# Performance work log

Measured on AMD Instinct MI355X. Metric: run time of the kernel, lower is better.

The kernel has to match this reference:

```python
import jax, jax.numpy as jnp
import numpy as np

L, KV, H, D, DM, F, V = 6, 1, 4, 256, 1152, 6912, 65536
HIST, T = 4095, 1
EPS = 1e-6


def setup_inputs():
    key = jax.random.key(0)
    ks = jax.random.split(key, 24)
    n = lambda k, s, sc=0.02: jax.random.normal(k, s, dtype=jnp.float32) * sc
    sf = D ** -0.25  # head_dim^-0.25 baked into q/k norm weights as in the source
    return {
        "input_ids": jax.random.randint(ks[0], (1, T), 0, V, dtype=jnp.int32),
        "attn_flag": 0,  # decode step: additive causal mask zeroed, as in the repo
        "key_cache": n(ks[1], (L, KV, D, HIST), 0.5),
        "value_cache": n(ks[2], (L, KV, HIST, D), 0.5),
        "embed_table": jax.random.randint(ks[3], (V, DM), 0, 256, dtype=jnp.int32),
        "embed_scale": jax.random.uniform(ks[4], (V, 1), minval=1e-4, maxval=1e-2, dtype=jnp.float32),
        "embed_zp": -jax.random.uniform(ks[5], (V, 1), minval=0.0, maxval=0.5, dtype=jnp.float32),
        "w_in_ln": 1.0 + n(ks[6], (L, DM)),
        "w_q_norm": (1.0 + n(ks[7], (L, D))) * sf,
        "w_k_norm": (1.0 + n(ks[8], (L, D))) * sf,
        "Wq": n(ks[9], (L, DM, H * D)),
        "Wk": n(ks[10], (L, DM, KV * D)),
        "Wv": n(ks[11], (L, DM, KV * D)),
        "Wo": n(ks[12], (L, H * D, DM)),
        "w_post_attn_ln": 1.0 + n(ks[13], (L, DM)),
        "w_pre_ffn_ln": 1.0 + n(ks[14], (L, DM)),
        "w_post_ffn_ln": 1.0 + n(ks[15], (L, DM)),
        "Wg": n(ks[16], (L, DM, F)),
        "Wu": n(ks[17], (L, DM, F)),
        "Wd": n(ks[18], (L, F, DM)),
        "w_final_norm": 1.0 + n(ks[19], (DM,)),
        "W_lm": n(ks[20], (DM, V)),
        "is_sliding": (jnp.arange(L) % 6) != 5,  # 5 local : 1 global pattern
    }


def _rms(x, w):
    return w * x / jnp.sqrt(jnp.mean(x * x, axis=-1, keepdims=True) + EPS)


def _rot_half(x, axis):
    x1, x2 = jnp.split(x, 2, axis=axis)
    return jnp.concatenate([-x2, x1], axis=axis)


def _rope(base, hist, S, d):
    pos = jnp.arange(hist, S, dtype=jnp.float32)[:, None]
    theta = base ** (-(jnp.arange(0, d, 2, dtype=jnp.float32) / d))
    ang = pos * theta
    c = jnp.concatenate([jnp.cos(ang)] * 2, axis=-1).astype(jnp.float16).astype(jnp.float32)
    s = jnp.concatenate([jnp.sin(ang)] * 2, axis=-1).astype(jnp.float16).astype(jnp.float32)
    return c, s  # (T, D), half-precision roundtrip mimics the .half() tables


def reference(input_ids, attn_flag, key_cache, value_cache, embed_table, embed_scale,
              embed_zp, w_in_ln, w_q_norm, w_k_norm, Wq, Wk, Wv, Wo, w_post_attn_ln,
              w_pre_ffn_ln, w_post_ffn_ln, Wg, Wu, Wd, w_final_norm, W_lm, is_sliding):
    Lc, KVc, Dd, hist = key_cache.shape
    Tq = input_ids.shape[1]
    S = hist + Tq
    Hh = Wq.shape[-1] // Dd
    G = Hh // KVc
    cos_g, sin_g = _rope(10000.0, hist, S, Dd)    # assigned to 'global' exactly as in source
    cos_l, sin_l = _rope(1000000.0, hist, S, Dd)  # assigned to 'local'
    mask = (jnp.arange(S)[None, :] > jnp.arange(Tq)[:, None]).astype(jnp.float32) * (-128.0 * float(attn_flag))  # (T,S)
    # int8-dequant embedding lookup: uint8 codes * per-row scale + per-row zero point
    h = embed_table[input_ids].astype(jnp.float32) * embed_scale[input_ids] + embed_zp[input_ids]  # (1,T,DM)

    def body(h, xs):
        ck, cv, slide, w_in, w_qn, w_kn, wq, wk, wv, wo, w_pa, w_pf, w_pof, wg, wu, wd = xs
        cq = jnp.where(slide, cos_l, cos_g)
        sq = jnp.where(slide, sin_l, sin_g)
        ckk, skk = cq.T, sq.T  # (D,T) for keys
        resid = h
        hn = _rms(h, w_in)                                                  # (1,T,DM)
        q = _rms((hn @ wq).reshape(Tq, Hh, Dd), w_qn).transpose(1, 0, 2)    # (H,T,D)
        k = _rms((hn @ wk).reshape(Tq, KVc, Dd), w_kn).transpose(1, 2, 0)   # (KV,D,T)
        v = (hn @ wv).reshape(Tq, KVc, Dd).transpose(1, 0, 2)               # (KV,T,D)
        q = q * cq + _rot_half(q, -1) * sq
        k = k * ckk[None] + _rot_half(k, 1) * skk[None]
        kf = jnp.concatenate([ck, k], axis=-1)   # (KV,D,S) new key cache
        vf = jnp.concatenate([cv, v], axis=1)    # (KV,S,D) new value cache
        kr = jnp.repeat(kf, G, axis=0)           # GQA repeat -> (H,D,S)
        vr = jnp.repeat(vf, G, axis=0)           # (H,S,D)
        attn = jax.nn.softmax(jnp.einsum('htd,hds->hts', q, kr) + mask[None], axis=-1)
        ao = jnp.einsum('hts,hsd->htd', attn, vr).transpose(1, 0, 2).reshape(1, Tq, Hh * Dd) @ wo
        h = resid + _rms(ao, w_pa)
        resid = h
        x = _rms(h, w_pf)
        m = (jax.nn.gelu(x @ wg, approximate=True) * (x @ wu)) @ wd
        h = resid + _rms(m, w_pof)
        return h, (kf, vf)

    h, (keys, values) = jax.lax.scan(
        body, h,
        (key_cache, value_cache, is_sliding, w_in_ln, w_q_norm, w_k_norm, Wq, Wk, Wv, Wo,
         w_post_attn_ln, w_pre_ffn_ln, w_post_ffn_ln, Wg, Wu, Wd))
    last = _rms(h[:, -1], w_final_norm)          # (1,DM)
    logits = last @ W_lm                          # (1,V)
    token = jnp.argmax(logits, axis=-1, keepdims=True).astype(jnp.int32)
    return keys, values, token
```

## Files before the change

kernel.cpp:

```cpp
#include <hip/hip_runtime.h>
#include <hip/hip_fp16.h>
#include <cmath>

#define LNUM 6
#define DM   1152
#define DHEAD 256
#define NH   4
#define FF   6912
#define VOC  65536
#define HIST 4095
#define SEQ  4096
#define EPSV 1e-6f

#define QKV_O 0
#define AP_O  9216
#define DP_O  16128
#define GU_O  23040
#define LG_O  105984
#define ZEND  171520
#define POP_O 171520
#define SPS_O 302592
#define HIN_O 303104
#define HM_O  310016
#define AMV_O 316928
#define AMI_O 317184

__device__ __forceinline__ float block_sum256(float v, float* red4) {
#pragma unroll
    for (int off = 32; off; off >>= 1) v += __shfl_xor(v, off);
    int t = threadIdx.x;
    if ((t & 63) == 0) red4[t >> 6] = v;
    __syncthreads();
    float r = red4[0] + red4[1] + red4[2] + red4[3];
    __syncthreads();
    return r;
}

__global__ __launch_bounds__(256) void gk_copy(const float* __restrict__ kc,
                                               const float* __restrict__ vc,
                                               float* __restrict__ keys,
                                               float* __restrict__ vals) {
    int b = blockIdx.x;
    if (b < 24576) {
        int row = b >> 4;
        int s = ((b & 15) << 8) + threadIdx.x;
        if (s < HIST) keys[(size_t)row * SEQ + s] = kc[(size_t)row * HIST + s];
    } else {
        int r = (b - 24576) * 4 + (threadIdx.x >> 6);
        int d4 = threadIdx.x & 63;
        if (r < LNUM * HIST) {
            int l = r / HIST, sI = r - l * HIST;
            ((float4*)(vals + ((size_t)l * SEQ + sI) * DHEAD))[d4] =
                ((const float4*)(vc + (size_t)r * DHEAD))[d4];
        }
    }
}

__global__ __launch_bounds__(256) void gk_qkv(
    const float* __restrict__ Wq, const float* __restrict__ Wk, const float* __restrict__ Wv,
    const float* __restrict__ w_in, const float* __restrict__ w_pof_prev,
    const float* __restrict__ hprev, const float* __restrict__ dprev,
    const int* __restrict__ ids, const int* __restrict__ tbl,
    const float* __restrict__ escale, const float* __restrict__ ezp,
    float* __restrict__ hin_out, float* __restrict__ qkv_out, int has_prev) {
    __shared__ float xv[DM];
    __shared__ float red4[4];
    __shared__ float4 qred[256];
    int t = threadIdx.x;
    if (has_prev) {
        float ss = 0.f;
        for (int i = t; i < DM; i += 256) { float d = dprev[i]; ss += d * d; }
        ss = block_sum256(ss, red4);
        float inv = 1.f / sqrtf(ss / DM + EPSV);
        for (int i = t; i < DM; i += 256)
            xv[i] = hprev[i] + w_pof_prev[i] * dprev[i] * inv;
    } else {
        int tok = ids[0];
        float sc = escale[tok], z = ezp[tok];
        const int* row = tbl + (size_t)tok * DM;
        for (int i = t; i < DM; i += 256) xv[i] = (float)row[i] * sc + z;
    }
    __syncthreads();
    if (blockIdx.x == 0 && blockIdx.y == 0)
        for (int i = t; i < DM; i += 256) hin_out[i] = xv[i];
    float ss = 0.f;
    for (int i = t; i < DM; i += 256) { float v = xv[i]; ss += v * v; }
    ss = block_sum256(ss, red4);
    float inv = 1.f / sqrtf(ss / DM + EPSV);
    for (int i = t; i < DM; i += 256) xv[i] = w_in[i] * xv[i] * inv;
    __syncthreads();

    int f4c = t & 63, ks = t >> 6;
    int jf = blockIdx.x * 64 + f4c;
    const float4* W4; int jj4, ncol4;
    if (jf < 256)      { W4 = (const float4*)Wq; jj4 = jf;       ncol4 = 256; }
    else if (jf < 320) { W4 = (const float4*)Wk; jj4 = jf - 256; ncol4 = 64; }
    else               { W4 = (const float4*)Wv; jj4 = jf - 320; ncol4 = 64; }
    int i0 = blockIdx.y * 64 + ks * 16;
    float4 w[16];
#pragma unroll
    for (int r = 0; r < 16; ++r) w[r] = W4[(size_t)(i0 + r) * ncol4 + jj4];
    float4 acc = {0, 0, 0, 0};
#pragma unroll
    for (int r = 0; r < 16; ++r) {
        float xs = xv[i0 + r];
        acc.x += xs * w[r].x; acc.y += xs * w[r].y;
        acc.z += xs * w[r].z; acc.w += xs * w[r].w;
    }
    qred[t] = acc;
    __syncthreads();
    if (ks == 0) {
        float4 a = qred[f4c], b = qred[64 + f4c], c = qred[128 + f4c], d = qred[192 + f4c];
        atomicAdd(&qkv_out[4 * jf + 0], a.x + b.x + c.x + d.x);
        atomicAdd(&qkv_out[4 * jf + 1], a.y + b.y + c.y + d.y);
        atomicAdd(&qkv_out[4 * jf + 2], a.z + b.z + c.z + d.z);
        atomicAdd(&qkv_out[4 * jf + 3], a.w + b.w + c.w + d.w);
    }
}

__global__ __launch_bounds__(256) void gk_attn(
    const float* __restrict__ qkv, const float* __restrict__ w_qn,
    const float* __restrict__ w_kn, const int* __restrict__ attn_flag,
    float* __restrict__ keys_l, float* __restrict__ vals_l,
    float* __restrict__ po_part, float* __restrict__ sum_part, float rope_base) {
    __shared__ float lq[NH * DHEAD];
    __shared__ float lqf[NH * DHEAD];
    __shared__ float lkn[DHEAD];
    __shared__ float lkf[DHEAD];
    __shared__ float lv[DHEAD];
    __shared__ float lp[NH * 32];
    __shared__ float red4[4];
    int t = threadIdx.x;
    int s0 = blockIdx.x * 32;
    bool last = (blockIdx.x == gridDim.x - 1);

    int jm = t & 127;
    float theta = powf(rope_base, -(float)(2 * jm) / 256.f);
    float ang = 4095.f * theta;
    float c = __half2float(__float2half(cosf(ang)));
    float s = __half2float(__float2half(sinf(ang)));

    for (int h = 0; h < NH; ++h) lq[h * 256 + t] = qkv[h * 256 + t];
    lkn[t] = qkv[1024 + t];
    lv[t]  = qkv[1280 + t];
    __syncthreads();
    for (int h = 0; h < NH; ++h) {
        float v = lq[h * 256 + t];
        float ss = block_sum256(v * v, red4);
        float inv = 1.f / sqrtf(ss / 256.f + EPSV);
        float qn = w_qn[t] * v * inv;
        lq[h * 256 + t] = qn;
        __syncthreads();
        float partner = (t < 128) ? -lq[h * 256 + t + 128] : lq[h * 256 + t - 128];
        lqf[h * 256 + t] = qn * c + partner * s;
    }
    {
        float v = lkn[t];
        float ss = block_sum256(v * v, red4);
        float inv = 1.f / sqrtf(ss / 256.f + EPSV);
        float kn = w_kn[t] * v * inv;
        lkn[t] = kn;
        __syncthreads();
        float partner = (t < 128) ? -lkn[t + 128] : lkn[t - 128];
        lkf[t] = kn * c + partner * s;
    }
    __syncthreads();
    if (last) {
        keys_l[(size_t)t * SEQ + (SEQ - 1)] = lkf[t];
        vals_l[(size_t)(SEQ - 1) * DHEAD + t] = lv[t];
    }
    int sl = t & 31, dc = t >> 5;
    int sg = s0 + sl;
    bool self = last && (sl == 31);
    float a0 = 0, a1 = 0, a2 = 0, a3 = 0;
#pragma unroll 4
    for (int dd = 0; dd < 32; ++dd) {
        int d = dc * 32 + dd;
        float kv = self ? lkf[d] : keys_l[(size_t)d * SEQ + sg];
        a0 += lqf[0 * 256 + d] * kv;
        a1 += lqf[1 * 256 + d] * kv;
        a2 += lqf[2 * 256 + d] * kv;
        a3 += lqf[3 * 256 + d] * kv;
    }
    __syncthreads();
    lq[0 * 256 + t] = a0; lq[1 * 256 + t] = a1; lq[2 * 256 + t] = a2; lq[3 * 256 + t] = a3;
    __syncthreads();
    if (t < 32) {
        int af = attn_flag[0];
        float mk = (s0 + t > 0) ? -128.f * (float)af : 0.f;
        for (int h = 0; h < NH; ++h) {
            float sc_ = 0.f;
#pragma unroll
            for (int d8 = 0; d8 < 8; ++d8) sc_ += lq[h * 256 + d8 * 32 + t];
            lp[h * 32 + t] = expf(sc_ + mk);
        }
    }
    __syncthreads();
    if (t < NH) {
        float su = 0.f;
        for (int i = 0; i < 32; ++i) su += lp[t * 32 + i];
        sum_part[blockIdx.x * NH + t] = su;
    }
    float p0 = 0, p1 = 0, p2 = 0, p3 = 0;
#pragma unroll 4
    for (int ss_ = 0; ss_ < 32; ++ss_) {
        float v = (last && ss_ == 31) ? lv[t] : vals_l[(size_t)(s0 + ss_) * DHEAD + t];
        p0 += lp[0 * 32 + ss_] * v;
        p1 += lp[1 * 32 + ss_] * v;
        p2 += lp[2 * 32 + ss_] * v;
        p3 += lp[3 * 32 + ss_] * v;
    }
    float* po = po_part + (size_t)blockIdx.x * NH * DHEAD;
    po[0 * 256 + t] = p0; po[1 * 256 + t] = p1; po[2 * 256 + t] = p2; po[3 * 256 + t] = p3;
}

__global__ __launch_bounds__(256) void gk_wo(
    const float* __restrict__ po_part, const float* __restrict__ sum_part,
    const float* __restrict__ Wo_l, float* __restrict__ aproj) {
    __shared__ float x[64];
    __shared__ float hinv[NH];
    __shared__ float red4[4];
    int t = threadIdx.x;
    for (int h = 0; h < NH; ++h) {
        float v = (t < 128) ? sum_part[t * NH + h] : 0.f;
        float tot = block_sum256(v, red4);
        if (t == 0) hinv[h] = 1.f / tot;
    }
    __syncthreads();
    int i0 = blockIdx.y * 64;
    if (t < 64) {
        float a = 0.f;
#pragma unroll 8
        for (int b = 0; b < 128; ++b) a += po_part[(size_t)b * 1024 + i0 + t];
        x[t] = a * hinv[(i0 + t) >> 8];
    }
    __syncthreads();
    int j = blockIdx.x * 256 + t;
    if (j < DM) {
        float acc = 0.f;
#pragma unroll 4
        for (int ii = 0; ii < 64; ++ii)
            acc += x[ii] * Wo_l[(size_t)(i0 + ii) * DM + j];
        atomicAdd(&aproj[j], acc);
    }
}

__global__ __launch_bounds__(256) void gk_gu(
    const float* __restrict__ Wg_l, const float* __restrict__ Wu_l,
    const float* __restrict__ w_pa, const float* __restrict__ w_pf,
    const float* __restrict__ hin, const float* __restrict__ aproj,
    float* __restrict__ hmid_out, float* __restrict__ gu_out) {
    __shared__ float xv[DM];
    __shared__ float red4[4];
    __shared__ float4 gred[256];
    int t = threadIdx.x;
    float ss = 0.f;
    for (int i = t; i < DM; i += 256) { float a = aproj[i]; ss += a * a; }
    ss = block_sum256(ss, red4);
    float inv = 1.f / sqrtf(ss / DM + EPSV);
    for (int i = t; i < DM; i += 256) xv[i] = hin[i] + w_pa[i] * aproj[i] * inv;
    __syncthreads();
    if (blockIdx.x == 0 && blockIdx.y == 0)
        for (int i = t; i < DM; i += 256) hmid_out[i] = xv[i];
    float s2 = 0.f;
    for (int i = t; i < DM; i += 256) { float v = xv[i]; s2 += v * v; }
    s2 = block_sum256(s2, red4);
    float inv2 = 1.f / sqrtf(s2 / DM + EPSV);
    for (int i = t; i < DM; i += 256) xv[i] = w_pf[i] * xv[i] * inv2;
    __syncthreads();

    int f4c = t & 63, ks = t >> 6;
    int cgi = blockIdx.x;
    bool isU = cgi >= 27;
    int cg = isU ? cgi - 27 : cgi;
    const float4* W4 = (const float4*)(isU ? Wu_l : Wg_l);
    int colf4 = cg * 64 + f4c;
    int i0 = blockIdx.y * 64 + ks * 16;
    float4 w[16];
#pragma unroll
    for (int r = 0; r < 16; ++r) w[r] = W4[(size_t)(i0 + r) * 1728 + colf4];
    float4 acc = {0, 0, 0, 0};
#pragma unroll
    for (int r = 0; r < 16; ++r) {
        float xs = xv[i0 + r];
        acc.x += xs * w[r].x; acc.y += xs * w[r].y;
        acc.z += xs * w[r].z; acc.w += xs * w[r].w;
    }
    gred[t] = acc;
    __syncthreads();
    if (ks == 0) {
        float4 a = gred[f4c], b = gred[64 + f4c], c = gred[128 + f4c], d = gred[192 + f4c];
        float* dst = gu_out + (isU ? FF : 0) + 4 * colf4;
        atomicAdd(dst + 0, a.x + b.x + c.x + d.x);
        atomicAdd(dst + 1, a.y + b.y + c.y + d.y);
        atomicAdd(dst + 2, a.z + b.z + c.z + d.z);
        atomicAdd(dst + 3, a.w + b.w + c.w + d.w);
    }
}

__global__ __launch_bounds__(256) void gk_wd(const float* __restrict__ gu,
                                             const float* __restrict__ Wd_l,
                                             float* __restrict__ dproj) {
    __shared__ float m[64];
    __shared__ float4 wred[256];
    int t = threadIdx.x;
    int i0 = blockIdx.y * 64;
    if (t < 64) {
        float g = gu[i0 + t], u = gu[FF + i0 + t];
        float gl = 0.5f * g * (1.f + tanhf(0.7978845608028654f * (g + 0.044715f * g * g * g)));
        m[t] = gl * u;
    }
    __syncthreads();
    int f4c = t & 63, ks = t >> 6;
    int col4 = blockIdx.x * 64 + f4c;
    float4 acc = {0, 0, 0, 0};
    if (col4 < 288) {
        const float4* W4 = (const float4*)Wd_l;
        float4 w[16];
#pragma unroll
        for (int r = 0; r < 16; ++r) w[r] = W4[(size_t)(i0 + ks * 16 + r) * 288 + col4];
#pragma unroll
        for (int r = 0; r < 16; ++r) {
            float xs = m[ks * 16 + r];
            acc.x += xs * w[r].x; acc.y += xs * w[r].y;
            acc.z += xs * w[r].z; acc.w += xs * w[r].w;
        }
    }
    wred[t] = acc;
    __syncthreads();
    if (ks == 0 && col4 < 288) {
        float4 a = wred[f4c], b = wred[64 + f4c], c = wred[128 + f4c], d = wred[192 + f4c];
        atomicAdd(&dproj[4 * col4 + 0], a.x + b.x + c.x + d.x);
        atomicAdd(&dproj[4 * col4 + 1], a.y + b.y + c.y + d.y);
        atomicAdd(&dproj[4 * col4 + 2], a.z + b.z + c.z + d.z);
        atomicAdd(&dproj[4 * col4 + 3], a.w + b.w + c.w + d.w);
    }
}

__global__ __launch_bounds__(256) void gk_logits(
    const float* __restrict__ W_lm, const float* __restrict__ w_pof5,
    const float* __restrict__ w_fin, const float* __restrict__ hmid5,
    const float* __restrict__ dproj5, float* __restrict__ lg) {
    __shared__ float xv[DM];
    __shared__ float red4[4];
    __shared__ float4 lred[256];
    int t = threadIdx.x;
    float ss = 0.f;
    for (int i = t; i < DM; i += 256) { float d = dproj5[i]; ss += d * d; }
    ss = block_sum256(ss, red4);
    float inv = 1.f / sqrtf(ss / DM + EPSV);
    for (int i = t; i < DM; i += 256) xv[i] = hmid5[i] + w_pof5[i] * dproj5[i] * inv;
    __syncthreads();
    float s2 = 0.f;
    for (int i = t; i < DM; i += 256) { float v = xv[i]; s2 += v * v; }
    s2 = block_sum256(s2, red4);
    float inv2 = 1.f / sqrtf(s2 / DM + EPSV);
    for (int i = t; i < DM; i += 256) xv[i] = w_fin[i] * xv[i] * inv2;
    __syncthreads();

    int f4c = t & 63, ks = t >> 6;
    int colf4 = blockIdx.x * 64 + f4c;
    int i0 = blockIdx.y * 64 + ks * 16;
    const float4* W4 = (const float4*)W_lm;
    float4 w[16];
#pragma unroll
    for (int r = 0; r < 16; ++r) w[r] = W4[(size_t)(i0 + r) * 16384 + colf4];
    float4 acc = {0, 0, 0, 0};
#pragma unroll
    for (int r = 0; r < 16; ++r) {
        float xs = xv[i0 + r];
        acc.x += xs * w[r].x; acc.y += xs * w[r].y;
        acc.z += xs * w[r].z; acc.w += xs * w[r].w;
    }
    lred[t] = acc;
    __syncthreads();
    if (ks == 0) {
        float4 a = lred[f4c], b = lred[64 + f4c], c = lred[128 + f4c], d = lred[192 + f4c];
        atomicAdd(&lg[4 * colf4 + 0], a.x + b.x + c.x + d.x);
        atomicAdd(&lg[4 * colf4 + 1], a.y + b.y + c.y + d.y);
        atomicAdd(&lg[4 * colf4 + 2], a.z + b.z + c.z + d.z);
        atomicAdd(&lg[4 * colf4 + 3], a.w + b.w + c.w + d.w);
    }
}

__global__ __launch_bounds__(256) void gk_amax1(const float* __restrict__ lg,
                                                float* __restrict__ pv, float* __restrict__ pi) {
    __shared__ float rv[256];
    __shared__ int ri[256];
    int t = threadIdx.x;
    int c = blockIdx.x * 256 + t;
    rv[t] = lg[c]; ri[t] = c;
    __syncthreads();
    for (int off = 128; off > 0; off >>= 1) {
        if (t < off) {
            float ov = rv[t + off]; int oi = ri[t + off];
            if (ov > rv[t] || (ov == rv[t] && oi < ri[t])) { rv[t] = ov; ri[t] = oi; }
        }
        __syncthreads();
    }
    if (t == 0) { pv[blockIdx.x] = rv[0]; pi[blockIdx.x] = (float)ri[0]; }
}

__global__ __launch_bounds__(256) void gk_amax2(const float* __restrict__ pv,
                                                const float* __restrict__ pi,
                                                float* __restrict__ tok_out) {
    __shared__ float rv[256];
    __shared__ int ri[256];
    int t = threadIdx.x;
    rv[t] = pv[t]; ri[t] = (int)pi[t];
    __syncthreads();
    for (int off = 128; off > 0; off >>= 1) {
        if (t < off) {
            float ov = rv[t + off]; int oi = ri[t + off];
            if (ov > rv[t] || (ov == rv[t] && oi < ri[t])) { rv[t] = ov; ri[t] = oi; }
        }
        __syncthreads();
    }
    if (t == 0) tok_out[0] = (float)ri[0];
}

extern "C" void kernel_launch(void* const* d_in, const int* in_sizes, int n_in,
                              void* d_out, int out_size, void* d_ws, size_t ws_size,
                              hipStream_t stream) {
    const int*   ids   = (const int*)d_in[0];
    const int*   aflag = (const int*)d_in[1];
    const float* kc    = (const float*)d_in[2];
    const float* vc    = (const float*)d_in[3];
    const int*   tbl   = (const int*)d_in[4];
    const float* esc   = (const float*)d_in[5];
    const float* ezp   = (const float*)d_in[6];
    const float* w_in  = (const float*)d_in[7];
    const float* w_qn  = (const float*)d_in[8];
    const float* w_kn  = (const float*)d_in[9];
    const float* Wq    = (const float*)d_in[10];
    const float* Wk    = (const float*)d_in[11];
    const float* Wv    = (const float*)d_in[12];
    const float* Wo    = (const float*)d_in[13];
    const float* w_pa  = (const float*)d_in[14];
    const float* w_pf  = (const float*)d_in[15];
    const float* w_pof = (const float*)d_in[16];
    const float* Wg    = (const float*)d_in[17];
    const float* Wu    = (const float*)d_in[18];
    const float* Wd    = (const float*)d_in[19];
    const float* w_fin = (const float*)d_in[20];
    const float* Wlm   = (const float*)d_in[21];

    float* keys = (float*)d_out;
    float* vals = keys + (size_t)LNUM * DHEAD * SEQ;
    float* tok  = vals + (size_t)LNUM * SEQ * DHEAD;
    float* ws = (float*)d_ws;

    hipMemsetAsync(ws, 0, ZEND * sizeof(float), stream);
    gk_copy<<<24576 + 6144, 256, 0, stream>>>(kc, vc, keys, vals);

    for (int l = 0; l < LNUM; ++l) {
        float* QKVl = ws + QKV_O + (size_t)l * 1536;
        float* APl  = ws + AP_O + (size_t)l * DM;
        float* DPl  = ws + DP_O + (size_t)l * DM;
        float* GUl  = ws + GU_O + (size_t)l * 2 * FF;
        float* HINl = ws + HIN_O + (size_t)l * DM;
        float* HMl  = ws + HM_O + (size_t)l * DM;
        float* keys_l = keys + (size_t)l * DHEAD * SEQ;
        float* vals_l = vals + (size_t)l * SEQ * DHEAD;

        gk_qkv<<<dim3(6, 18), 256, 0, stream>>>(
            Wq + (size_t)l * DM * 1024, Wk + (size_t)l * DM * 256,
            Wv + (size_t)l * DM * 256, w_in + (size_t)l * DM,
            w_pof + (size_t)(l ? l - 1 : 0) * DM,
            (l ? ws + HM_O + (size_t)(l - 1) * DM : nullptr),
            (l ? ws + DP_O + (size_t)(l - 1) * DM : nullptr),
            ids, tbl, esc, ezp, HINl, QKVl, (l > 0) ? 1 : 0);

        gk_attn<<<128, 256, 0, stream>>>(
            QKVl, w_qn + (size_t)l * DHEAD, w_kn + (size_t)l * DHEAD,
            aflag, keys_l, vals_l, ws + POP_O, ws + SPS_O,
            ((l % 6) != 5) ? 1000000.0f : 10000.0f);

        gk_wo<<<dim3(5, 16), 256, 0, stream>>>(
            ws + POP_O, ws + SPS_O, Wo + (size_t)l * 1024 * DM, APl);

        gk_gu<<<dim3(54, 18), 256, 0, stream>>>(
            Wg + (size_t)l * DM * FF, Wu + (size_t)l * DM * FF,
            w_pa + (size_t)l * DM, w_pf + (size_t)l * DM, HINl, APl, HMl, GUl);

        gk_wd<<<dim3(5, 108), 256, 0, stream>>>(GUl, Wd + (size_t)l * FF * DM, DPl);
    }

    gk_logits<<<dim3(256, 18), 256, 0, stream>>>(
        Wlm, w_pof + (size_t)5 * DM, w_fin,
        ws + HM_O + (size_t)5 * DM, ws + DP_O + (size_t)5 * DM, ws + LG_O);
    gk_amax1<<<256, 256, 0, stream>>>(ws + LG_O, ws + AMV_O, ws + AMI_O);
    gk_amax2<<<1, 256, 0, stream>>>(ws + AMV_O, ws + AMI_O, tok);
}
```

Before: 579.1 us.

## Replace atomic split-K reductions with partial buffers summed by consumers

```diff
diff --git a/kernel.cpp b/kernel.cpp
--- a/kernel.cpp
+++ b/kernel.cpp
@@ -12,18 +12,18 @@
 #define SEQ  4096
 #define EPSV 1e-6f
 
-#define QKV_O 0
-#define AP_O  9216
-#define DP_O  16128
-#define GU_O  23040
-#define LG_O  105984
-#define ZEND  171520
-#define POP_O 171520
-#define SPS_O 302592
-#define HIN_O 303104
-#define HM_O  310016
-#define AMV_O 316928
-#define AMI_O 317184
+#define POP_O   0
+#define SPS_O   131072
+#define QKVP_O  131584
+#define APP_O   159232
+#define DPP_O   177664
+#define GUP_O   302080
+#define LGP_O   550912
+#define HIN_O   944128
+#define HM_O    951040
+#define XL_O    957952
+#define AMX_O   959104
+#define CNT_O   959106
 
 __device__ __forceinline__ float block_sum256(float v, float* red4) {
 #pragma unroll
@@ -58,36 +58,41 @@
 
 __global__ __launch_bounds__(256) void gk_qkv(
     const float* __restrict__ Wq, const float* __restrict__ Wk, const float* __restrict__ Wv,
-    const float* __restrict__ w_in, const float* __restrict__ w_pof_prev,
-    const float* __restrict__ hprev, const float* __restrict__ dprev,
+    const float* __restrict__ wln, const float* __restrict__ wres,
+    const float* __restrict__ hbase, const float* __restrict__ dpp,
     const int* __restrict__ ids, const int* __restrict__ tbl,
-    const float* __restrict__ escale, const float* __restrict__ ezp,
-    float* __restrict__ hin_out, float* __restrict__ qkv_out, int has_prev) {
+    const float* __restrict__ esc, const float* __restrict__ ezp,
+    float* __restrict__ hin_out, float* __restrict__ qkvp, int has_prev) {
     __shared__ float xv[DM];
     __shared__ float red4[4];
     __shared__ float4 qred[256];
     int t = threadIdx.x;
     if (has_prev) {
+        for (int i = t; i < DM; i += 256) {
+            float d = 0.f;
+#pragma unroll 4
+            for (int p2 = 0; p2 < 108; ++p2) d += dpp[p2 * DM + i];
+            xv[i] = d;
+        }
         float ss = 0.f;
-        for (int i = t; i < DM; i += 256) { float d = dprev[i]; ss += d * d; }
+        for (int i = t; i < DM; i += 256) { float d = xv[i]; ss += d * d; }
         ss = block_sum256(ss, red4);
         float inv = 1.f / sqrtf(ss / DM + EPSV);
         for (int i = t; i < DM; i += 256)
-            xv[i] = hprev[i] + w_pof_prev[i] * dprev[i] * inv;
+            xv[i] = hbase[i] + wres[i] * xv[i] * inv;
     } else {
         int tok = ids[0];
-        float sc = escale[tok], z = ezp[tok];
+        float sc = esc[tok], z = ezp[tok];
         const int* row = tbl + (size_t)tok * DM;
         for (int i = t; i < DM; i += 256) xv[i] = (float)row[i] * sc + z;
     }
-    __syncthreads();
     if (blockIdx.x == 0 && blockIdx.y == 0)
         for (int i = t; i < DM; i += 256) hin_out[i] = xv[i];
-    float ss = 0.f;
-    for (int i = t; i < DM; i += 256) { float v = xv[i]; ss += v * v; }
-    ss = block_sum256(ss, red4);
-    float inv = 1.f / sqrtf(ss / DM + EPSV);
-    for (int i = t; i < DM; i += 256) xv[i] = w_in[i] * xv[i] * inv;
+    float s2 = 0.f;
+    for (int i = t; i < DM; i += 256) { float v = xv[i]; s2 += v * v; }
+    s2 = block_sum256(s2, red4);
+    float inv2 = 1.f / sqrtf(s2 / DM + EPSV);
+    for (int i = t; i < DM; i += 256) xv[i] = wln[i] * xv[i] * inv2;
     __syncthreads();
 
     int f4c = t & 63, ks = t >> 6;
@@ -111,15 +116,16 @@
     __syncthreads();
     if (ks == 0) {
         float4 a = qred[f4c], b = qred[64 + f4c], c = qred[128 + f4c], d = qred[192 + f4c];
-        atomicAdd(&qkv_out[4 * jf + 0], a.x + b.x + c.x + d.x);
-        atomicAdd(&qkv_out[4 * jf + 1], a.y + b.y + c.y + d.y);
-        atomicAdd(&qkv_out[4 * jf + 2], a.z + b.z + c.z + d.z);
-        atomicAdd(&qkv_out[4 * jf + 3], a.w + b.w + c.w + d.w);
+        float* dst = qkvp + (size_t)blockIdx.y * 1536 + 4 * jf;
+        dst[0] = a.x + b.x + c.x + d.x;
+        dst[1] = a.y + b.y + c.y + d.y;
+        dst[2] = a.z + b.z + c.z + d.z;
+        dst[3] = a.w + b.w + c.w + d.w;
     }
 }
 
 __global__ __launch_bounds__(256) void gk_attn(
-    const float* __restrict__ qkv, const float* __restrict__ w_qn,
+    const float* __restrict__ qkvp, const float* __restrict__ w_qn,
     const float* __restrict__ w_kn, const int* __restrict__ attn_flag,
     float* __restrict__ keys_l, float* __restrict__ vals_l,
     float* __restrict__ po_part, float* __restrict__ sum_part, float rope_base) {
@@ -129,7 +135,6 @@
     __shared__ float lkf[DHEAD];
     __shared__ float lv[DHEAD];
     __shared__ float lp[NH * 32];
-    __shared__ float red4[4];
     int t = threadIdx.x;
     int s0 = blockIdx.x * 32;
     bool last = (blockIdx.x == gridDim.x - 1);
@@ -140,29 +145,44 @@
     float c = __half2float(__float2half(cosf(ang)));
     float s = __half2float(__float2half(sinf(ang)));
 
-    for (int h = 0; h < NH; ++h) lq[h * 256 + t] = qkv[h * 256 + t];
-    lkn[t] = qkv[1024 + t];
-    lv[t]  = qkv[1280 + t];
-    __syncthreads();
-    for (int h = 0; h < NH; ++h) {
-        float v = lq[h * 256 + t];
-        float ss = block_sum256(v * v, red4);
-        float inv = 1.f / sqrtf(ss / 256.f + EPSV);
-        float qn = w_qn[t] * v * inv;
-        lq[h * 256 + t] = qn;
-        __syncthreads();
-        float partner = (t < 128) ? -lq[h * 256 + t + 128] : lq[h * 256 + t - 128];
-        lqf[h * 256 + t] = qn * c + partner * s;
-    }
+    for (int j = t; j < 1536; j += 256) {
+        float v = 0.f;
+#pragma unroll
+        for (int p2 = 0; p2 < 18; ++p2) v += qkvp[p2 * 1536 + j];
+        if (j < 1024) lq[j] = v;
+        else if (j < 1280) lkn[j - 1024] = v;
+        else lv[j - 1280] = v;
+    }
+    __syncthreads();
+    int wv = t >> 6, ln = t & 63;
+    float sq = 0.f, sk = 0.f;
+#pragma unroll
+    for (int j = 0; j < 4; ++j) {
+        float v = lq[wv * 256 + j * 64 + ln]; sq += v * v;
+        float u = lkn[j * 64 + ln];           sk += u * u;
+    }
+#pragma unroll
+    for (int off = 32; off; off >>= 1) { sq += __shfl_xor(sq, off); sk += __shfl_xor(sk, off); }
+    float invq = 1.f / sqrtf(sq / 256.f + EPSV);
+    float invk = 1.f / sqrtf(sk / 256.f + EPSV);
+    __syncthreads();
+#pragma unroll
+    for (int j = 0; j < 4; ++j) {
+        int d = j * 64 + ln;
+        lq[wv * 256 + d] *= w_qn[d] * invq;
+        if (wv == 0) lkn[d] *= w_kn[d] * invk;
+    }
+    __syncthreads();
     {
-        float v = lkn[t];
-        float ss = block_sum256(v * v, red4);
-        float inv = 1.f / sqrtf(ss / 256.f + EPSV);
-        float kn = w_kn[t] * v * inv;
-        lkn[t] = kn;
-        __syncthreads();
-        float partner = (t < 128) ? -lkn[t + 128] : lkn[t - 128];
-        lkf[t] = kn * c + partner * s;
+        float kn = lkn[t];
+        float prk = (t < 128) ? -lkn[t + 128] : lkn[t - 128];
+        lkf[t] = kn * c + prk * s;
+#pragma unroll
+        for (int h = 0; h < NH; ++h) {
+            float qn = lq[h * 256 + t];
+            float pr = (t < 128) ? -lq[h * 256 + t + 128] : lq[h * 256 + t - 128];
+            lqf[h * 256 + t] = qn * c + pr * s;
+        }
     }
     __syncthreads();
     if (last) {
@@ -216,7 +236,7 @@
 
 __global__ __launch_bounds__(256) void gk_wo(
     const float* __restrict__ po_part, const float* __restrict__ sum_part,
-    const float* __restrict__ Wo_l, float* __restrict__ aproj) {
+    const float* __restrict__ Wo_l, float* __restrict__ app) {
     __shared__ float x[64];
     __shared__ float hinv[NH];
     __shared__ float red4[4];
@@ -241,27 +261,32 @@
 #pragma unroll 4
         for (int ii = 0; ii < 64; ++ii)
             acc += x[ii] * Wo_l[(size_t)(i0 + ii) * DM + j];
-        atomicAdd(&aproj[j], acc);
+        app[(size_t)blockIdx.y * DM + j] = acc;
     }
 }
 
 __global__ __launch_bounds__(256) void gk_gu(
     const float* __restrict__ Wg_l, const float* __restrict__ Wu_l,
     const float* __restrict__ w_pa, const float* __restrict__ w_pf,
-    const float* __restrict__ hin, const float* __restrict__ aproj,
-    float* __restrict__ hmid_out, float* __restrict__ gu_out) {
+    const float* __restrict__ hin, const float* __restrict__ app,
+    float* __restrict__ hm_out, float* __restrict__ gup) {
     __shared__ float xv[DM];
     __shared__ float red4[4];
     __shared__ float4 gred[256];
     int t = threadIdx.x;
+    for (int i = t; i < DM; i += 256) {
+        float a = 0.f;
+#pragma unroll
+        for (int p2 = 0; p2 < 16; ++p2) a += app[p2 * DM + i];
+        xv[i] = a;
+    }
     float ss = 0.f;
-    for (int i = t; i < DM; i += 256) { float a = aproj[i]; ss += a * a; }
+    for (int i = t; i < DM; i += 256) { float a = xv[i]; ss += a * a; }
     ss = block_sum256(ss, red4);
     float inv = 1.f / sqrtf(ss / DM + EPSV);
-    for (int i = t; i < DM; i += 256) xv[i] = hin[i] + w_pa[i] * aproj[i] * inv;
-    __syncthreads();
+    for (int i = t; i < DM; i += 256) xv[i] = hin[i] + w_pa[i] * xv[i] * inv;
     if (blockIdx.x == 0 && blockIdx.y == 0)
-        for (int i = t; i < DM; i += 256) hmid_out[i] = xv[i];
+        for (int i = t; i < DM; i += 256) hm_out[i] = xv[i];
     float s2 = 0.f;
     for (int i = t; i < DM; i += 256) { float v = xv[i]; s2 += v * v; }
     s2 = block_sum256(s2, red4);
@@ -290,23 +315,28 @@
     __syncthreads();
     if (ks == 0) {
         float4 a = gred[f4c], b = gred[64 + f4c], c = gred[128 + f4c], d = gred[192 + f4c];
-        float* dst = gu_out + (isU ? FF : 0) + 4 * colf4;
-        atomicAdd(dst + 0, a.x + b.x + c.x + d.x);
-        atomicAdd(dst + 1, a.y + b.y + c.y + d.y);
-        atomicAdd(dst + 2, a.z + b.z + c.z + d.z);
-        atomicAdd(dst + 3, a.w + b.w + c.w + d.w);
-    }
-}
-
-__global__ __launch_bounds__(256) void gk_wd(const float* __restrict__ gu,
+        float* dst = gup + (size_t)blockIdx.y * 13824 + (isU ? FF : 0) + 4 * colf4;
+        dst[0] = a.x + b.x + c.x + d.x;
+        dst[1] = a.y + b.y + c.y + d.y;
+        dst[2] = a.z + b.z + c.z + d.z;
+        dst[3] = a.w + b.w + c.w + d.w;
+    }
+}
+
+__global__ __launch_bounds__(256) void gk_wd(const float* __restrict__ gup,
                                              const float* __restrict__ Wd_l,
-                                             float* __restrict__ dproj) {
+                                             float* __restrict__ dpp) {
     __shared__ float m[64];
     __shared__ float4 wred[256];
     int t = threadIdx.x;
     int i0 = blockIdx.y * 64;
     if (t < 64) {
-        float g = gu[i0 + t], u = gu[FF + i0 + t];
+        float g = 0.f, u = 0.f;
+#pragma unroll
+        for (int p2 = 0; p2 < 18; ++p2) {
+            g += gup[(size_t)p2 * 13824 + i0 + t];
+            u += gup[(size_t)p2 * 13824 + FF + i0 + t];
+        }
         float gl = 0.5f * g * (1.f + tanhf(0.7978845608028654f * (g + 0.044715f * g * g * g)));
         m[t] = gl * u;
     }
@@ -330,93 +360,102 @@
     __syncthreads();
     if (ks == 0 && col4 < 288) {
         float4 a = wred[f4c], b = wred[64 + f4c], c = wred[128 + f4c], d = wred[192 + f4c];
-        atomicAdd(&dproj[4 * col4 + 0], a.x + b.x + c.x + d.x);
-        atomicAdd(&dproj[4 * col4 + 1], a.y + b.y + c.y + d.y);
-        atomicAdd(&dproj[4 * col4 + 2], a.z + b.z + c.z + d.z);
-        atomicAdd(&dproj[4 * col4 + 3], a.w + b.w + c.w + d.w);
-    }
-}
-
-__global__ __launch_bounds__(256) void gk_logits(
-    const float* __restrict__ W_lm, const float* __restrict__ w_pof5,
-    const float* __restrict__ w_fin, const float* __restrict__ hmid5,
-    const float* __restrict__ dproj5, float* __restrict__ lg) {
+        float* dst = dpp + (size_t)blockIdx.y * DM + 4 * col4;
+        dst[0] = a.x + b.x + c.x + d.x;
+        dst[1] = a.y + b.y + c.y + d.y;
+        dst[2] = a.z + b.z + c.z + d.z;
+        dst[3] = a.w + b.w + c.w + d.w;
+    }
+}
+
+__global__ __launch_bounds__(256) void gk_prepL(
+    const float* __restrict__ hm5, const float* __restrict__ dpp,
+    const float* __restrict__ wpof5, const float* __restrict__ wfin,
+    float* __restrict__ xl, unsigned long long* __restrict__ amx,
+    unsigned int* __restrict__ cnt) {
     __shared__ float xv[DM];
     __shared__ float red4[4];
-    __shared__ float4 lred[256];
-    int t = threadIdx.x;
+    int t = threadIdx.x;
+    for (int i = t; i < DM; i += 256) {
+        float d = 0.f;
+#pragma unroll 4
+        for (int p2 = 0; p2 < 108; ++p2) d += dpp[p2 * DM + i];
+        xv[i] = d;
+    }
     float ss = 0.f;
-    for (int i = t; i < DM; i += 256) { float d = dproj5[i]; ss += d * d; }
+    for (int i = t; i < DM; i += 256) { float d = xv[i]; ss += d * d; }
     ss = block_sum256(ss, red4);
     float inv = 1.f / sqrtf(ss / DM + EPSV);
-    for (int i = t; i < DM; i += 256) xv[i] = hmid5[i] + w_pof5[i] * dproj5[i] * inv;
-    __syncthreads();
+    for (int i = t; i < DM; i += 256) xv[i] = hm5[i] + wpof5[i] * xv[i] * inv;
     float s2 = 0.f;
     for (int i = t; i < DM; i += 256) { float v = xv[i]; s2 += v * v; }
     s2 = block_sum256(s2, red4);
     float inv2 = 1.f / sqrtf(s2 / DM + EPSV);
-    for (int i = t; i < DM; i += 256) xv[i] = w_fin[i] * xv[i] * inv2;
-    __syncthreads();
-
+    for (int i = t; i < DM; i += 256) xl[i] = wfin[i] * xv[i] * inv2;
+    if (t == 0) { *amx = 0ull; *cnt = 0u; }
+}
+
+__global__ __launch_bounds__(256) void gk_logits(
+    const float* __restrict__ W_lm, const float* __restrict__ xl,
+    float* __restrict__ lgp) {
+    __shared__ float4 lred[256];
+    int t = threadIdx.x;
     int f4c = t & 63, ks = t >> 6;
     int colf4 = blockIdx.x * 64 + f4c;
-    int i0 = blockIdx.y * 64 + ks * 16;
     const float4* W4 = (const float4*)W_lm;
-    float4 w[16];
-#pragma unroll
-    for (int r = 0; r < 16; ++r) w[r] = W4[(size_t)(i0 + r) * 16384 + colf4];
     float4 acc = {0, 0, 0, 0};
 #pragma unroll
-    for (int r = 0; r < 16; ++r) {
-        float xs = xv[i0 + r];
-        acc.x += xs * w[r].x; acc.y += xs * w[r].y;
-        acc.z += xs * w[r].z; acc.w += xs * w[r].w;
+    for (int bb = 0; bb < 3; ++bb) {
+        int i0 = blockIdx.y * 192 + ks * 48 + bb * 16;
+        float4 w[16];
+#pragma unroll
+        for (int r = 0; r < 16; ++r) w[r] = W4[(size_t)(i0 + r) * 16384 + colf4];
+#pragma unroll
+        for (int r = 0; r < 16; ++r) {
+            float xs = xl[i0 + r];
+            acc.x += xs * w[r].x; acc.y += xs * w[r].y;
+            acc.z += xs * w[r].z; acc.w += xs * w[r].w;
+        }
     }
     lred[t] = acc;
     __syncthreads();
     if (ks == 0) {
         float4 a = lred[f4c], b = lred[64 + f4c], c = lred[128 + f4c], d = lred[192 + f4c];
-        atomicAdd(&lg[4 * colf4 + 0], a.x + b.x + c.x + d.x);
-        atomicAdd(&lg[4 * colf4 + 1], a.y + b.y + c.y + d.y);
-        atomicAdd(&lg[4 * colf4 + 2], a.z + b.z + c.z + d.z);
-        atomicAdd(&lg[4 * colf4 + 3], a.w + b.w + c.w + d.w);
-    }
-}
-
-__global__ __launch_bounds__(256) void gk_amax1(const float* __restrict__ lg,
-                                                float* __restrict__ pv, float* __restrict__ pi) {
-    __shared__ float rv[256];
-    __shared__ int ri[256];
+        float* dst = lgp + (size_t)blockIdx.y * VOC + 4 * colf4;
+        dst[0] = a.x + b.x + c.x + d.x;
+        dst[1] = a.y + b.y + c.y + d.y;
+        dst[2] = a.z + b.z + c.z + d.z;
+        dst[3] = a.w + b.w + c.w + d.w;
+    }
+}
+
+__global__ __launch_bounds__(256) void gk_amax(
+    const float* __restrict__ lgp, unsigned long long* __restrict__ amx,
+    unsigned int* __restrict__ cnt, float* __restrict__ tok_out) {
+    __shared__ unsigned long long smu[256];
     int t = threadIdx.x;
     int c = blockIdx.x * 256 + t;
-    rv[t] = lg[c]; ri[t] = c;
-    __syncthreads();
-    for (int off = 128; off > 0; off >>= 1) {
-        if (t < off) {
-            float ov = rv[t + off]; int oi = ri[t + off];
-            if (ov > rv[t] || (ov == rv[t] && oi < ri[t])) { rv[t] = ov; ri[t] = oi; }
-        }
+    float v = 0.f;
+#pragma unroll
+    for (int p2 = 0; p2 < 6; ++p2) v += lgp[(size_t)p2 * VOC + c];
+    unsigned bits = __float_as_uint(v);
+    unsigned key = (bits & 0x80000000u) ? ~bits : (bits | 0x80000000u);
+    smu[t] = ((unsigned long long)key << 32) | (unsigned)(~c);
+    __syncthreads();
+    for (int off = 128; off; off >>= 1) {
+        if (t < off) { if (smu[t + off] > smu[t]) smu[t] = smu[t + off]; }
         __syncthreads();
     }
-    if (t == 0) { pv[blockIdx.x] = rv[0]; pi[blockIdx.x] = (float)ri[0]; }
-}
-
-__global__ __launch_bounds__(256) void gk_amax2(const float* __restrict__ pv,
-                                                const float* __restrict__ pi,
-                                                float* __restrict__ tok_out) {
-    __shared__ float rv[256];
-    __shared__ int ri[256];
-    int t = threadIdx.x;
-    rv[t] = pv[t]; ri[t] = (int)pi[t];
-    __syncthreads();
-    for (int off = 128; off > 0; off >>= 1) {
-        if (t < off) {
-            float ov = rv[t + off]; int oi = ri[t + off];
-            if (ov > rv[t] || (ov == rv[t] && oi < ri[t])) { rv[t] = ov; ri[t] = oi; }
-        }
-        __syncthreads();
-    }
-    if (t == 0) tok_out[0] = (float)ri[0];
+    if (t == 0) {
+        atomicMax(amx, smu[0]);
+        __threadfence();
+        unsigned tk = atomicAdd(cnt, 1u);
+        if (tk == 255u) {
+            unsigned long long fin = atomicMax(amx, 0ull);
+            unsigned cc = ~(unsigned)(fin & 0xFFFFFFFFull);
+            tok_out[0] = (float)cc;
+        }
+    }
 }
 
 extern "C" void kernel_launch(void* const* d_in, const int* in_sizes, int n_in,
@@ -450,45 +489,48 @@
     float* tok  = vals + (size_t)LNUM * SEQ * DHEAD;
     float* ws = (float*)d_ws;
 
-    hipMemsetAsync(ws, 0, ZEND * sizeof(float), stream);
     gk_copy<<<24576 + 6144, 256, 0, stream>>>(kc, vc, keys, vals);
 
     for (int l = 0; l < LNUM; ++l) {
-        float* QKVl = ws + QKV_O + (size_t)l * 1536;
-        float* APl  = ws + AP_O + (size_t)l * DM;
-        float* DPl  = ws + DP_O + (size_t)l * DM;
-        float* GUl  = ws + GU_O + (size_t)l * 2 * FF;
-        float* HINl = ws + HIN_O + (size_t)l * DM;
-        float* HMl  = ws + HM_O + (size_t)l * DM;
         float* keys_l = keys + (size_t)l * DHEAD * SEQ;
         float* vals_l = vals + (size_t)l * SEQ * DHEAD;
 
         gk_qkv<<<dim3(6, 18), 256, 0, stream>>>(
             Wq + (size_t)l * DM * 1024, Wk + (size_t)l * DM * 256,
-            Wv + (size_t)l * DM * 256, w_in + (size_t)l * DM,
-            w_pof + (size_t)(l ? l - 1 : 0) * DM,
+            Wv + (size_t)l * DM * 256,
+            w_in + (size_t)l * DM,
+            (l ? w_pof + (size_t)(l - 1) * DM : w_in),
             (l ? ws + HM_O + (size_t)(l - 1) * DM : nullptr),
-            (l ? ws + DP_O + (size_t)(l - 1) * DM : nullptr),
-            ids, tbl, esc, ezp, HINl, QKVl, (l > 0) ? 1 : 0);
+            ws + DPP_O,
+            ids, tbl, esc, ezp,
+            ws + HIN_O + (size_t)l * DM, ws + QKVP_O, (l > 0) ? 1 : 0);
 
         gk_attn<<<128, 256, 0, stream>>>(
-            QKVl, w_qn + (size_t)l * DHEAD, w_kn + (size_t)l * DHEAD,
+            ws + QKVP_O, w_qn + (size_t)l * DHEAD, w_kn + (size_t)l * DHEAD,
             aflag, keys_l, vals_l, ws + POP_O, ws + SPS_O,
             ((l % 6) != 5) ? 1000000.0f : 10000.0f);
 
         gk_wo<<<dim3(5, 16), 256, 0, stream>>>(
-            ws + POP_O, ws + SPS_O, Wo + (size_t)l * 1024 * DM, APl);
+            ws + POP_O, ws + SPS_O, Wo + (size_t)l * 1024 * DM, ws + APP_O);
 
         gk_gu<<<dim3(54, 18), 256, 0, stream>>>(
             Wg + (size_t)l * DM * FF, Wu + (size_t)l * DM * FF,
-            w_pa + (size_t)l * DM, w_pf + (size_t)l * DM, HINl, APl, HMl, GUl);
-
-        gk_wd<<<dim3(5, 108), 256, 0, stream>>>(GUl, Wd + (size_t)l * FF * DM, DPl);
-    }
-
-    gk_logits<<<dim3(256, 18), 256, 0, stream>>>(
-        Wlm, w_pof + (size_t)5 * DM, w_fin,
-        ws + HM_O + (size_t)5 * DM, ws + DP_O + (size_t)5 * DM, ws + LG_O);
-    gk_amax1<<<256, 256, 0, stream>>>(ws + LG_O, ws + AMV_O, ws + AMI_O);
-    gk_amax2<<<1, 256, 0, stream>>>(ws + AMV_O, ws + AMI_O, tok);
-}
+            w_pa + (size_t)l * DM, w_pf + (size_t)l * DM,
+            ws + HIN_O + (size_t)l * DM, ws + APP_O,
+            ws + HM_O + (size_t)l * DM, ws + GUP_O);
+
+        gk_wd<<<dim3(5, 108), 256, 0, stream>>>(
+            ws + GUP_O, Wd + (size_t)l * FF * DM, ws + DPP_O);
+    }
+
+    gk_prepL<<<1, 256, 0, stream>>>(
+        ws + HM_O + (size_t)5 * DM, ws + DPP_O,
+        w_pof + (size_t)5 * DM, w_fin, ws + XL_O,
+        (unsigned long long*)(ws + AMX_O), (unsigned int*)(ws + CNT_O));
+
+    gk_logits<<<dim3(256, 6), 256, 0, stream>>>(Wlm, ws + XL_O, ws + LGP_O);
+
+    gk_amax<<<256, 256, 0, stream>>>(
+        ws + LGP_O, (unsigned long long*)(ws + AMX_O),
+        (unsigned int*)(ws + CNT_O), tok);
+}
```

New measurement: 788.5 us. +36.1%, slower.
